# Kernel optimization log

Hardware: AMD Instinct MI355X
Metric: run time of the kernel (lower is better)

The kernel has to match this reference:

```python
import jax, jax.numpy as jnp
import numpy as np

N_NODES = 50000
N_EDGES = 800000
DIM_IN, DIM_H, DIM_OUT = 128, 128, 64


def _init_linear(key, fan_in, fan_out):
    # kaiming-uniform-ish init, matches torch Linear scale
    lim = 1.0 / np.sqrt(fan_in)
    return jax.random.uniform(key, (fan_in, fan_out), jnp.float32, -lim, lim)


def setup_inputs() -> dict:
    key = jax.random.key(0)
    ks = jax.random.split(key, 12)
    x = jax.random.normal(ks[0], (N_NODES, DIM_IN), jnp.float32)
    edge_index = jax.random.randint(ks[1], (2, N_EDGES), 0, N_NODES, jnp.int32)
    dims = [(DIM_IN, DIM_H), (DIM_H, DIM_H), (DIM_H, DIM_OUT)]
    inp = {"x": x, "edge_index": edge_index}
    for i, (fi, fo) in enumerate(dims):
        inp[f"Wl{i}"] = _init_linear(ks[2 + 3 * i], fi, fo)   # neighbor transform
        inp[f"Wr{i}"] = _init_linear(ks[3 + 3 * i], fi, fo)   # root transform
        inp[f"b{i}"] = jnp.zeros((fo,), jnp.float32)
    return inp


def _sage_layer(x, src, dst, Wl, Wr, b):
    # mean aggregation of neighbor messages x[src] at destination nodes
    msg = x[src]                                              # [E, d]
    agg = jax.ops.segment_sum(msg, dst, num_segments=N_NODES)  # [N, d]
    cnt = jax.ops.segment_sum(jnp.ones((src.shape[0],), x.dtype), dst,
                              num_segments=N_NODES)
    mean = agg / jnp.maximum(cnt, 1.0)[:, None]               # isolated nodes -> 0
    return mean @ Wl + b + x @ Wr                              # SAGEConv


def reference(x, edge_index, Wl0, Wr0, b0, Wl1, Wr1, b1, Wl2, Wr2, b2):
    src, dst = edge_index[0], edge_index[1]
    layers = [(Wl0, Wr0, b0), (Wl1, Wr1, b1), (Wl2, Wr2, b2)]
    h = x
    for i, (Wl, Wr, b) in enumerate(layers):
        h = _sage_layer(h, src, dst, Wl, Wr, b)
        if i != len(layers) - 1:
            h = jax.nn.relu(h)  # dropout p=0.2 is identity in eval mode
    return jax.nn.log_softmax(h, axis=1), h
```

## Files before the change

kernel.cpp:

```cpp
#include <hip/hip_runtime.h>

#define N_NODES 50000
#define N_EDGES 800000
#define SCAN_BLOCKS 196
#define WIN 6250

typedef __attribute__((ext_vector_type(8))) short short8;
typedef __attribute__((ext_vector_type(4))) float f32x4;
typedef unsigned short ushort_t;
typedef unsigned int uint_t;

__device__ inline ushort_t f2bf(float f) {
    union { float f; uint_t u; } v; v.f = f;
    uint_t u = v.u;
    u += 0x7fffu + ((u >> 16) & 1u);
    return (ushort_t)(u >> 16);
}
__device__ inline float bflo(uint_t v) { return __uint_as_float(v << 16); }
__device__ inline float bfhi(uint_t v) { return __uint_as_float(v & 0xffff0000u); }
__device__ inline uint_t packbf(float a, float b) {
    return (uint_t)f2bf(a) | ((uint_t)f2bf(b) << 16);
}

__global__ void prep(const float* __restrict__ x, uint_t* __restrict__ x_bf_u,
                     const float* __restrict__ Wl0, const float* __restrict__ Wr0,
                     const float* __restrict__ Wl1, const float* __restrict__ Wr1,
                     const float* __restrict__ Wl2, const float* __restrict__ Wr2,
                     ushort_t* __restrict__ pk0, ushort_t* __restrict__ pk1,
                     ushort_t* __restrict__ pkz, int* __restrict__ cnt) {
    int b = blockIdx.x, tid = threadIdx.x;
    if (b < 6250) {
        int i = b * 256 + tid;
        float4 v = ((const float4*)x)[i];
        x_bf_u[i * 2] = packbf(v.x, v.y);
        x_bf_u[i * 2 + 1] = packbf(v.z, v.w);
    } else if (b < 6506) {
        int bb = b - 6250;
        const float* Wl = (bb < 128) ? Wl0 : Wl1;
        const float* Wr = (bb < 128) ? Wr0 : Wr1;
        ushort_t* out = (bb < 128) ? pk0 : pk1;
        int idx = (bb & 127) * 256 + tid;
        int j = idx & 7, l = (idx >> 3) & 63, t = (idx >> 9) & 7, ks = idx >> 12;
        int n = t * 16 + (l & 15);
        int k = ks * 32 + (l >> 4) * 8 + j;
        float w = (k < 128) ? Wl[k * 128 + n] : Wr[(k - 128) * 128 + n];
        out[idx] = f2bf(w);
    } else if (b < 6570) {
        int idx = (b - 6506) * 256 + tid;
        int j = idx & 7, l = (idx >> 3) & 63, t = (idx >> 9) & 7, ks = idx >> 12;
        int n = t * 16 + (l & 15);
        int k = ks * 32 + (l >> 4) * 8 + j;
        float w = (n < 64) ? Wl2[k * 64 + n] : Wr2[k * 64 + (n - 64)];
        pkz[idx] = f2bf(w);
    } else {
        int i = (b - 6570) * 256 + tid;
        if (i < 12500) ((int4*)cnt)[i] = make_int4(0, 0, 0, 0);
    }
}

__global__ void count_edges_mp(const int* __restrict__ ei, int* __restrict__ cnt) {
    int g = blockIdx.x & 7;
    int nb = gridDim.x >> 3;
    int bi = blockIdx.x >> 3;
    int lo = g * WIN;
    for (int e = bi * 256 + threadIdx.x; e < N_EDGES; e += nb * 256) {
        int d = ei[N_EDGES + e];
        if ((unsigned)(d - lo) < WIN) atomicAdd(&cnt[d], 1);
    }
}

__global__ void fill_csr_mp(const int* __restrict__ ei, int* __restrict__ cursor,
                            int* __restrict__ csr_src) {
    int g = blockIdx.x & 7;
    int nb = gridDim.x >> 3;
    int bi = blockIdx.x >> 3;
    int lo = g * WIN;
    for (int e = bi * 256 + threadIdx.x; e < N_EDGES; e += nb * 256) {
        int d = ei[N_EDGES + e];
        if ((unsigned)(d - lo) < WIN) {
            int p = atomicAdd(&cursor[d], 1);
            csr_src[p] = ei[e];
        }
    }
}

__global__ void scan_all(const int* __restrict__ cnt, int* __restrict__ rowstart,
                         int* __restrict__ cursor) {
    __shared__ int s[256];
    __shared__ int wsum[4];
    int t = threadIdx.x, b = blockIdx.x;
    int base = b * 256;
    int pre = 0;
    for (int i = t; i < base; i += 256) pre += cnt[i];
    for (int off = 32; off; off >>= 1) pre += __shfl_down(pre, off, 64);
    if ((t & 63) == 0) wsum[t >> 6] = pre;
    __syncthreads();
    int prefix_base = wsum[0] + wsum[1] + wsum[2] + wsum[3];
    int i = base + t;
    int v = (i < N_NODES) ? cnt[i] : 0;
    s[t] = v;
    __syncthreads();
    for (int off = 1; off < 256; off <<= 1) {
        int add = (t >= off) ? s[t - off] : 0;
        __syncthreads();
        s[t] += add;
        __syncthreads();
    }
    int excl = s[t] - v + prefix_base;
    if (i < N_NODES) { rowstart[i] = excl; cursor[i] = excl; }
    if (b == 0 && t == 0) rowstart[N_NODES] = N_EDGES;
}

__device__ inline void gather_mean4_128(const uint4* __restrict__ base,
                                        const int* __restrict__ rowstart,
                                        const int* __restrict__ csr,
                                        int node, int lane, float* acc) {
    int s0 = rowstart[node], s1 = rowstart[node + 1];
    #pragma unroll
    for (int k = 0; k < 8; ++k) acc[k] = 0.f;
    int chunk = lane & 15, esel = lane >> 4;
    for (int b = s0; b < s1; b += 64) {
        int m = min(64, s1 - b);
        int idx = (lane < m) ? csr[b + lane] : 0;
        int j = 0;
        for (; j + 16 <= m; j += 16) {
            int i0 = __shfl(idx, j + esel, 64);
            int i1 = __shfl(idx, j + 4 + esel, 64);
            int i2 = __shfl(idx, j + 8 + esel, 64);
            int i3 = __shfl(idx, j + 12 + esel, 64);
            uint4 v0 = base[(size_t)i0 * 16 + chunk];
            uint4 v1 = base[(size_t)i1 * 16 + chunk];
            uint4 v2 = base[(size_t)i2 * 16 + chunk];
            uint4 v3 = base[(size_t)i3 * 16 + chunk];
            acc[0] += (bflo(v0.x) + bflo(v1.x)) + (bflo(v2.x) + bflo(v3.x));
            acc[1] += (bfhi(v0.x) + bfhi(v1.x)) + (bfhi(v2.x) + bfhi(v3.x));
            acc[2] += (bflo(v0.y) + bflo(v1.y)) + (bflo(v2.y) + bflo(v3.y));
            acc[3] += (bfhi(v0.y) + bfhi(v1.y)) + (bfhi(v2.y) + bfhi(v3.y));
            acc[4] += (bflo(v0.z) + bflo(v1.z)) + (bflo(v2.z) + bflo(v3.z));
            acc[5] += (bfhi(v0.z) + bfhi(v1.z)) + (bfhi(v2.z) + bfhi(v3.z));
            acc[6] += (bflo(v0.w) + bflo(v1.w)) + (bflo(v2.w) + bflo(v3.w));
            acc[7] += (bfhi(v0.w) + bfhi(v1.w)) + (bfhi(v2.w) + bfhi(v3.w));
        }
        for (; j < m; j += 4) {
            int e = j + esel;
            int s = __shfl(idx, min(e, m - 1), 64);
            if (e < m) {
                uint4 v = base[(size_t)s * 16 + chunk];
                acc[0] += bflo(v.x); acc[1] += bfhi(v.x);
                acc[2] += bflo(v.y); acc[3] += bfhi(v.y);
                acc[4] += bflo(v.z); acc[5] += bfhi(v.z);
                acc[6] += bflo(v.w); acc[7] += bfhi(v.w);
            }
        }
    }
    float inv = 1.0f / fmaxf((float)(s1 - s0), 1.0f);
    #pragma unroll
    for (int k = 0; k < 8; ++k) {
        acc[k] += __shfl_xor(acc[k], 16, 64);
        acc[k] += __shfl_xor(acc[k], 32, 64);
        acc[k] *= inv;
    }
}

template <bool CHAIN>
__global__ __launch_bounds__(512, 8) void layer_fused(
    const uint4* __restrict__ gsrc, const ushort_t* __restrict__ root,
    const int* __restrict__ rowstart, const int* __restrict__ csr_src,
    const ushort_t* __restrict__ Bpk, const float* __restrict__ bias1,
    const ushort_t* __restrict__ Bpkz, const float* __restrict__ bias2,
    ushort_t* __restrict__ h_out,
    ushort_t* __restrict__ z_bf, float* __restrict__ r_f32) {
    __shared__ __align__(16) ushort_t At[16 * 136];
    int lane = threadIdx.x & 63, wave = threadIdx.x >> 6;
    int nodeBase = blockIdx.x * 16;
    int chunk = lane & 15;

    #pragma unroll
    for (int i = 0; i < 2; ++i) {
        int m = wave * 2 + i;
        int node = nodeBase + m;
        float acc[8];
        #pragma unroll
        for (int k = 0; k < 8; ++k) acc[k] = 0.f;
        if (node < N_NODES) gather_mean4_128(gsrc, rowstart, csr_src, node, lane, acc);
        if (lane < 16) {
            uint4 w;
            w.x = packbf(acc[0], acc[1]); w.y = packbf(acc[2], acc[3]);
            w.z = packbf(acc[4], acc[5]); w.w = packbf(acc[6], acc[7]);
            *(uint4*)&At[m * 136 + chunk * 8] = w;
        }
    }
    __syncthreads();

    int row16 = lane & 15, quad = lane >> 4;
    const short8* bp = (const short8*)Bpk + lane;
    int rootRow = min(nodeBase + row16, N_NODES - 1);
    const ushort_t* rrow = root + (size_t)rootRow * 128;

    f32x4 acc1 = {0.f, 0.f, 0.f, 0.f};
    #pragma unroll
    for (int ks = 0; ks < 8; ++ks) {
        short8 afrag;
        if (ks < 4) afrag = *(const short8*)&At[row16 * 136 + ks * 32 + quad * 8];
        else        afrag = *(const short8*)(rrow + (ks - 4) * 32 + quad * 8);
        short8 bfrag = bp[(ks * 8 + wave) * 64];
        acc1 = __builtin_amdgcn_mfma_f32_16x16x32_bf16(afrag, bfrag, acc1, 0, 0, 0);
    }

    int col = wave * 16 + row16;
    if (!CHAIN) {
        float bv = bias1[col];
        #pragma unroll
        for (int r = 0; r < 4; ++r) {
            int row = nodeBase + quad * 4 + r;
            if (row < N_NODES) {
                float v = fmaxf(acc1[r] + bv, 0.f);
                h_out[(size_t)row * 128 + col] = f2bf(v);
            }
        }
    } else {
        __syncthreads();
        float bv = bias1[col];
        #pragma unroll
        for (int r = 0; r < 4; ++r) {
            float v = fmaxf(acc1[r] + bv, 0.f);
            At[(quad * 4 + r) * 136 + col] = f2bf(v);
        }
        __syncthreads();

        const short8* bpz = (const short8*)Bpkz + lane;
        f32x4 acc2 = {0.f, 0.f, 0.f, 0.f};
        #pragma unroll
        for (int ks = 0; ks < 4; ++ks) {
            short8 afrag = *(const short8*)&At[row16 * 136 + ks * 32 + quad * 8];
            short8 bfrag = bpz[(ks * 8 + wave) * 64];
            acc2 = __builtin_amdgcn_mfma_f32_16x16x32_bf16(afrag, bfrag, acc2, 0, 0, 0);
        }

        #pragma unroll
        for (int r = 0; r < 4; ++r) {
            int row = nodeBase + quad * 4 + r;
            if (row < N_NODES) {
                if (col < 64) z_bf[(size_t)row * 64 + col] = f2bf(acc2[r]);
                else          r_f32[(size_t)row * 64 + (col - 64)] = acc2[r] + bias2[col - 64];
            }
        }
    }
}

__global__ void final_agg_softmax(const uint4* __restrict__ zb,
                                  const float* __restrict__ r_f32,
                                  const int* __restrict__ rowstart,
                                  const int* __restrict__ csr_src,
                                  float* __restrict__ out) {
    int node = blockIdx.x * 4 + (threadIdx.x >> 6);
    int lane = threadIdx.x & 63;
    if (node >= N_NODES) return;
    int s0 = rowstart[node], s1 = rowstart[node + 1];
    int chunk = lane & 7, esel = lane >> 3;
    float acc[8];
    #pragma unroll
    for (int k = 0; k < 8; ++k) acc[k] = 0.f;
    for (int b = s0; b < s1; b += 64) {
        int m = min(64, s1 - b);
        int idx = (lane < m) ? csr_src[b + lane] : 0;
        int j = 0;
        for (; j + 32 <= m; j += 32) {
            int i0 = __shfl(idx, j + esel, 64);
            int i1 = __shfl(idx, j + 8 + esel, 64);
            int i2 = __shfl(idx, j + 16 + esel, 64);
            int i3 = __shfl(idx, j + 24 + esel, 64);
            uint4 v0 = zb[(size_t)i0 * 8 + chunk];
            uint4 v1 = zb[(size_t)i1 * 8 + chunk];
            uint4 v2 = zb[(size_t)i2 * 8 + chunk];
            uint4 v3 = zb[(size_t)i3 * 8 + chunk];
            acc[0] += (bflo(v0.x) + bflo(v1.x)) + (bflo(v2.x) + bflo(v3.x));
            acc[1] += (bfhi(v0.x) + bfhi(v1.x)) + (bfhi(v2.x) + bfhi(v3.x));
            acc[2] += (bflo(v0.y) + bflo(v1.y)) + (bflo(v2.y) + bflo(v3.y));
            acc[3] += (bfhi(v0.y) + bfhi(v1.y)) + (bfhi(v2.y) + bfhi(v3.y));
            acc[4] += (bflo(v0.z) + bflo(v1.z)) + (bflo(v2.z) + bflo(v3.z));
            acc[5] += (bfhi(v0.z) + bfhi(v1.z)) + (bfhi(v2.z) + bfhi(v3.z));
            acc[6] += (bflo(v0.w) + bflo(v1.w)) + (bflo(v2.w) + bflo(v3.w));
            acc[7] += (bfhi(v0.w) + bfhi(v1.w)) + (bfhi(v2.w) + bfhi(v3.w));
        }
        for (; j < m; j += 8) {
            int e = j + esel;
            int s = __shfl(idx, min(e, m - 1), 64);
            if (e < m) {
                uint4 v = zb[(size_t)s * 8 + chunk];
                acc[0] += bflo(v.x); acc[1] += bfhi(v.x);
                acc[2] += bflo(v.y); acc[3] += bfhi(v.y);
                acc[4] += bflo(v.z); acc[5] += bfhi(v.z);
                acc[6] += bflo(v.w); acc[7] += bfhi(v.w);
            }
        }
    }
    float inv = 1.0f / fmaxf((float)(s1 - s0), 1.0f);
    #pragma unroll
    for (int k = 0; k < 8; ++k) {
        acc[k] += __shfl_xor(acc[k], 8, 64);
        acc[k] += __shfl_xor(acc[k], 16, 64);
        acc[k] += __shfl_xor(acc[k], 32, 64);
    }
    const float4* rp = (const float4*)(r_f32 + (size_t)node * 64 + chunk * 8);
    float4 r0 = rp[0], r1 = rp[1];
    float h[8];
    h[0] = acc[0] * inv + r0.x; h[1] = acc[1] * inv + r0.y;
    h[2] = acc[2] * inv + r0.z; h[3] = acc[3] * inv + r0.w;
    h[4] = acc[4] * inv + r1.x; h[5] = acc[5] * inv + r1.y;
    h[6] = acc[6] * inv + r1.z; h[7] = acc[7] * inv + r1.w;
    float mx = h[0];
    #pragma unroll
    for (int k = 1; k < 8; ++k) mx = fmaxf(mx, h[k]);
    mx = fmaxf(mx, __shfl_xor(mx, 1, 64));
    mx = fmaxf(mx, __shfl_xor(mx, 2, 64));
    mx = fmaxf(mx, __shfl_xor(mx, 4, 64));
    float s = 0.f;
    #pragma unroll
    for (int k = 0; k < 8; ++k) s += expf(h[k] - mx);
    s += __shfl_xor(s, 1, 64);
    s += __shfl_xor(s, 2, 64);
    s += __shfl_xor(s, 4, 64);
    float lse = mx + logf(s);
    if (lane < 8) {
        float4* o0 = (float4*)(out + (size_t)node * 64 + chunk * 8);
        float4* o1 = (float4*)(out + (size_t)N_NODES * 64 + (size_t)node * 64 + chunk * 8);
        float4 a = {h[0] - lse, h[1] - lse, h[2] - lse, h[3] - lse};
        float4 bq = {h[4] - lse, h[5] - lse, h[6] - lse, h[7] - lse};
        o0[0] = a; o0[1] = bq;
        float4 c = {h[0], h[1], h[2], h[3]};
        float4 d = {h[4], h[5], h[6], h[7]};
        o1[0] = c; o1[1] = d;
    }
}

extern "C" void kernel_launch(void* const* d_in, const int* in_sizes, int n_in,
                              void* d_out, int out_size, void* d_ws, size_t ws_size,
                              hipStream_t stream) {
    const float* x  = (const float*)d_in[0];
    const int* ei   = (const int*)d_in[1];
    const float* Wl0 = (const float*)d_in[2];
    const float* Wr0 = (const float*)d_in[3];
    const float* b0  = (const float*)d_in[4];
    const float* Wl1 = (const float*)d_in[5];
    const float* Wr1 = (const float*)d_in[6];
    const float* b1  = (const float*)d_in[7];
    const float* Wl2 = (const float*)d_in[8];
    const float* Wr2 = (const float*)d_in[9];
    const float* b2  = (const float*)d_in[10];
    float* out = (float*)d_out;

    char* ws = (char*)d_ws;
    int* cnt      = (int*)(ws + 0x000000);
    int* rowstart = (int*)(ws + 0x040000);
    int* cursor   = (int*)(ws + 0x080000);
    int* csr_src  = (int*)(ws + 0x100000);
    ushort_t* pk0 = (ushort_t*)(ws + 0x420000);
    ushort_t* pk1 = (ushort_t*)(ws + 0x440000);
    ushort_t* pkz = (ushort_t*)(ws + 0x460000);
    ushort_t* x_bf = (ushort_t*)(ws + 0x0500000);
    ushort_t* h1   = (ushort_t*)(ws + 0x1F00000);
    ushort_t* z_bf = (ushort_t*)(ws + 0x1200000);
    float*    r_f32 = (float*)  (ws + 0x0500000);

    prep<<<6619, 256, 0, stream>>>(x, (uint_t*)x_bf, Wl0, Wr0, Wl1, Wr1, Wl2, Wr2,
                                   pk0, pk1, pkz, cnt);

    count_edges_mp<<<1024, 256, 0, stream>>>(ei, cnt);
    scan_all<<<SCAN_BLOCKS, 256, 0, stream>>>(cnt, rowstart, cursor);
    fill_csr_mp<<<1024, 256, 0, stream>>>(ei, cursor, csr_src);

    layer_fused<false><<<3125, 512, 0, stream>>>(
        (const uint4*)x_bf, x_bf, rowstart, csr_src, pk0, b0,
        nullptr, nullptr, h1, nullptr, nullptr);

    layer_fused<true><<<3125, 512, 0, stream>>>(
        (const uint4*)h1, h1, rowstart, csr_src, pk1, b1,
        pkz, b2, nullptr, z_bf, r_f32);

    final_agg_softmax<<<12500, 256, 0, stream>>>((const uint4*)z_bf, r_f32,
                                                 rowstart, csr_src, out);
}
```

Baseline: 337.4 us.

## Gather neighbor features in FP8 instead of BF16 across all three layers

Adds FP8 (e4m3) copies of x, the layer-1 output and the final-layer z projection. All neighbor-gather loops read these 1-byte values instead of BF16, halving the bytes fetched per edge in the memory-bound aggregation. Each lane now handles 16 features, so lane mapping and shuffle reductions are reworked, and the fused layer's launch-bounds occupancy hint drops from 8 to 4. The cost is extra byte-granular stores for the FP8 copies and a noticeable accuracy loss, since values are cast to FP8 without any scaling.

```diff
diff --git a/kernel.cpp b/kernel.cpp
--- a/kernel.cpp
+++ b/kernel.cpp
@@ -7,6 +7,7 @@
 
 typedef __attribute__((ext_vector_type(8))) short short8;
 typedef __attribute__((ext_vector_type(4))) float f32x4;
+typedef __attribute__((ext_vector_type(2))) float f32x2;
 typedef unsigned short ushort_t;
 typedef unsigned int uint_t;
 
@@ -16,13 +17,24 @@
     u += 0x7fffu + ((u >> 16) & 1u);
     return (ushort_t)(u >> 16);
 }
-__device__ inline float bflo(uint_t v) { return __uint_as_float(v << 16); }
-__device__ inline float bfhi(uint_t v) { return __uint_as_float(v & 0xffff0000u); }
 __device__ inline uint_t packbf(float a, float b) {
     return (uint_t)f2bf(a) | ((uint_t)f2bf(b) << 16);
 }
+__device__ inline void acc_fp8x4(uint_t u, float* a) {
+    f32x2 p0 = __builtin_amdgcn_cvt_pk_f32_fp8(u, false);
+    f32x2 p1 = __builtin_amdgcn_cvt_pk_f32_fp8(u, true);
+    a[0] += p0.x; a[1] += p0.y; a[2] += p1.x; a[3] += p1.y;
+}
+__device__ inline void acc_fp8x16(uint4 v, float* a) {
+    acc_fp8x4(v.x, a); acc_fp8x4(v.y, a + 4);
+    acc_fp8x4(v.z, a + 8); acc_fp8x4(v.w, a + 12);
+}
+__device__ inline unsigned char f2fp8(float f) {
+    return (unsigned char)(__builtin_amdgcn_cvt_pk_fp8_f32(f, f, 0, false) & 0xff);
+}
 
 __global__ void prep(const float* __restrict__ x, uint_t* __restrict__ x_bf_u,
+                     uint_t* __restrict__ x_f8_u,
                      const float* __restrict__ Wl0, const float* __restrict__ Wr0,
                      const float* __restrict__ Wl1, const float* __restrict__ Wr1,
                      const float* __restrict__ Wl2, const float* __restrict__ Wr2,
@@ -34,6 +46,9 @@
         float4 v = ((const float4*)x)[i];
         x_bf_u[i * 2] = packbf(v.x, v.y);
         x_bf_u[i * 2 + 1] = packbf(v.z, v.w);
+        uint_t u = __builtin_amdgcn_cvt_pk_fp8_f32(v.x, v.y, 0, false);
+        u = __builtin_amdgcn_cvt_pk_fp8_f32(v.z, v.w, u, true);
+        x_f8_u[i] = u;
     } else if (b < 6506) {
         int bb = b - 6250;
         const float* Wl = (bb < 128) ? Wl0 : Wl1;
@@ -111,51 +126,37 @@
     if (b == 0 && t == 0) rowstart[N_NODES] = N_EDGES;
 }
 
-__device__ inline void gather_mean4_128(const uint4* __restrict__ base,
-                                        const int* __restrict__ rowstart,
-                                        const int* __restrict__ csr,
-                                        int node, int lane, float* acc) {
+__device__ inline void gather_mean_fp8_128(const uint4* __restrict__ base,
+                                           const int* __restrict__ rowstart,
+                                           const int* __restrict__ csr,
+                                           int node, int lane, float* acc) {
     int s0 = rowstart[node], s1 = rowstart[node + 1];
-    #pragma unroll
-    for (int k = 0; k < 8; ++k) acc[k] = 0.f;
-    int chunk = lane & 15, esel = lane >> 4;
+    int chunk = lane & 7, esel = lane >> 3;
     for (int b = s0; b < s1; b += 64) {
         int m = min(64, s1 - b);
         int idx = (lane < m) ? csr[b + lane] : 0;
         int j = 0;
         for (; j + 16 <= m; j += 16) {
             int i0 = __shfl(idx, j + esel, 64);
-            int i1 = __shfl(idx, j + 4 + esel, 64);
-            int i2 = __shfl(idx, j + 8 + esel, 64);
-            int i3 = __shfl(idx, j + 12 + esel, 64);
-            uint4 v0 = base[(size_t)i0 * 16 + chunk];
-            uint4 v1 = base[(size_t)i1 * 16 + chunk];
-            uint4 v2 = base[(size_t)i2 * 16 + chunk];
-            uint4 v3 = base[(size_t)i3 * 16 + chunk];
-            acc[0] += (bflo(v0.x) + bflo(v1.x)) + (bflo(v2.x) + bflo(v3.x));
-            acc[1] += (bfhi(v0.x) + bfhi(v1.x)) + (bfhi(v2.x) + bfhi(v3.x));
-            acc[2] += (bflo(v0.y) + bflo(v1.y)) + (bflo(v2.y) + bflo(v3.y));
-            acc[3] += (bfhi(v0.y) + bfhi(v1.y)) + (bfhi(v2.y) + bfhi(v3.y));
-            acc[4] += (bflo(v0.z) + bflo(v1.z)) + (bflo(v2.z) + bflo(v3.z));
-            acc[5] += (bfhi(v0.z) + bfhi(v1.z)) + (bfhi(v2.z) + bfhi(v3.z));
-            acc[6] += (bflo(v0.w) + bflo(v1.w)) + (bflo(v2.w) + bflo(v3.w));
-            acc[7] += (bfhi(v0.w) + bfhi(v1.w)) + (bfhi(v2.w) + bfhi(v3.w));
-        }
-        for (; j < m; j += 4) {
+            int i1 = __shfl(idx, j + 8 + esel, 64);
+            uint4 v0 = base[(size_t)i0 * 8 + chunk];
+            uint4 v1 = base[(size_t)i1 * 8 + chunk];
+            acc_fp8x16(v0, acc);
+            acc_fp8x16(v1, acc);
+        }
+        for (; j < m; j += 8) {
             int e = j + esel;
             int s = __shfl(idx, min(e, m - 1), 64);
             if (e < m) {
-                uint4 v = base[(size_t)s * 16 + chunk];
-                acc[0] += bflo(v.x); acc[1] += bfhi(v.x);
-                acc[2] += bflo(v.y); acc[3] += bfhi(v.y);
-                acc[4] += bflo(v.z); acc[5] += bfhi(v.z);
-                acc[6] += bflo(v.w); acc[7] += bfhi(v.w);
+                uint4 v = base[(size_t)s * 8 + chunk];
+                acc_fp8x16(v, acc);
             }
         }
     }
     float inv = 1.0f / fmaxf((float)(s1 - s0), 1.0f);
     #pragma unroll
-    for (int k = 0; k < 8; ++k) {
+    for (int k = 0; k < 16; ++k) {
+        acc[k] += __shfl_xor(acc[k], 8, 64);
         acc[k] += __shfl_xor(acc[k], 16, 64);
         acc[k] += __shfl_xor(acc[k], 32, 64);
         acc[k] *= inv;
@@ -163,31 +164,35 @@
 }
 
 template <bool CHAIN>
-__global__ __launch_bounds__(512, 8) void layer_fused(
-    const uint4* __restrict__ gsrc, const ushort_t* __restrict__ root,
+__global__ __launch_bounds__(512, 4) void layer_fused(
+    const uint4* __restrict__ gsrc_f8, const ushort_t* __restrict__ root,
     const int* __restrict__ rowstart, const int* __restrict__ csr_src,
     const ushort_t* __restrict__ Bpk, const float* __restrict__ bias1,
     const ushort_t* __restrict__ Bpkz, const float* __restrict__ bias2,
-    ushort_t* __restrict__ h_out,
-    ushort_t* __restrict__ z_bf, float* __restrict__ r_f32) {
+    ushort_t* __restrict__ h_out, unsigned char* __restrict__ h_out_f8,
+    unsigned char* __restrict__ z_f8, float* __restrict__ r_f32) {
     __shared__ __align__(16) ushort_t At[16 * 136];
     int lane = threadIdx.x & 63, wave = threadIdx.x >> 6;
     int nodeBase = blockIdx.x * 16;
-    int chunk = lane & 15;
+    int chunk = lane & 7;
 
     #pragma unroll
     for (int i = 0; i < 2; ++i) {
         int m = wave * 2 + i;
         int node = nodeBase + m;
-        float acc[8];
-        #pragma unroll
-        for (int k = 0; k < 8; ++k) acc[k] = 0.f;
-        if (node < N_NODES) gather_mean4_128(gsrc, rowstart, csr_src, node, lane, acc);
-        if (lane < 16) {
-            uint4 w;
-            w.x = packbf(acc[0], acc[1]); w.y = packbf(acc[2], acc[3]);
-            w.z = packbf(acc[4], acc[5]); w.w = packbf(acc[6], acc[7]);
-            *(uint4*)&At[m * 136 + chunk * 8] = w;
+        float acc[16];
+        #pragma unroll
+        for (int k = 0; k < 16; ++k) acc[k] = 0.f;
+        if (node < N_NODES)
+            gather_mean_fp8_128(gsrc_f8, rowstart, csr_src, node, lane, acc);
+        if (lane < 8) {
+            uint4 w0, w1;
+            w0.x = packbf(acc[0], acc[1]);  w0.y = packbf(acc[2], acc[3]);
+            w0.z = packbf(acc[4], acc[5]);  w0.w = packbf(acc[6], acc[7]);
+            w1.x = packbf(acc[8], acc[9]);  w1.y = packbf(acc[10], acc[11]);
+            w1.z = packbf(acc[12], acc[13]); w1.w = packbf(acc[14], acc[15]);
+            *(uint4*)&At[m * 136 + chunk * 16] = w0;
+            *(uint4*)&At[m * 136 + chunk * 16 + 8] = w1;
         }
     }
     __syncthreads();
@@ -216,6 +221,7 @@
             if (row < N_NODES) {
                 float v = fmaxf(acc1[r] + bv, 0.f);
                 h_out[(size_t)row * 128 + col] = f2bf(v);
+                h_out_f8[(size_t)row * 128 + col] = f2fp8(v);
             }
         }
     } else {
@@ -241,14 +247,14 @@
         for (int r = 0; r < 4; ++r) {
             int row = nodeBase + quad * 4 + r;
             if (row < N_NODES) {
-                if (col < 64) z_bf[(size_t)row * 64 + col] = f2bf(acc2[r]);
+                if (col < 64) z_f8[(size_t)row * 64 + col] = f2fp8(acc2[r]);
                 else          r_f32[(size_t)row * 64 + (col - 64)] = acc2[r] + bias2[col - 64];
             }
         }
     }
 }
 
-__global__ void final_agg_softmax(const uint4* __restrict__ zb,
+__global__ void final_agg_softmax(const uint4* __restrict__ zb_f8,
                                   const float* __restrict__ r_f32,
                                   const int* __restrict__ rowstart,
                                   const int* __restrict__ csr_src,
@@ -257,80 +263,72 @@
     int lane = threadIdx.x & 63;
     if (node >= N_NODES) return;
     int s0 = rowstart[node], s1 = rowstart[node + 1];
-    int chunk = lane & 7, esel = lane >> 3;
-    float acc[8];
-    #pragma unroll
-    for (int k = 0; k < 8; ++k) acc[k] = 0.f;
+    int chunk = lane & 3, esel = lane >> 2;
+    float acc[16];
+    #pragma unroll
+    for (int k = 0; k < 16; ++k) acc[k] = 0.f;
     for (int b = s0; b < s1; b += 64) {
         int m = min(64, s1 - b);
         int idx = (lane < m) ? csr_src[b + lane] : 0;
         int j = 0;
         for (; j + 32 <= m; j += 32) {
             int i0 = __shfl(idx, j + esel, 64);
-            int i1 = __shfl(idx, j + 8 + esel, 64);
-            int i2 = __shfl(idx, j + 16 + esel, 64);
-            int i3 = __shfl(idx, j + 24 + esel, 64);
-            uint4 v0 = zb[(size_t)i0 * 8 + chunk];
-            uint4 v1 = zb[(size_t)i1 * 8 + chunk];
-            uint4 v2 = zb[(size_t)i2 * 8 + chunk];
-            uint4 v3 = zb[(size_t)i3 * 8 + chunk];
-            acc[0] += (bflo(v0.x) + bflo(v1.x)) + (bflo(v2.x) + bflo(v3.x));
-            acc[1] += (bfhi(v0.x) + bfhi(v1.x)) + (bfhi(v2.x) + bfhi(v3.x));
-            acc[2] += (bflo(v0.y) + bflo(v1.y)) + (bflo(v2.y) + bflo(v3.y));
-            acc[3] += (bfhi(v0.y) + bfhi(v1.y)) + (bfhi(v2.y) + bfhi(v3.y));
-            acc[4] += (bflo(v0.z) + bflo(v1.z)) + (bflo(v2.z) + bflo(v3.z));
-            acc[5] += (bfhi(v0.z) + bfhi(v1.z)) + (bfhi(v2.z) + bfhi(v3.z));
-            acc[6] += (bflo(v0.w) + bflo(v1.w)) + (bflo(v2.w) + bflo(v3.w));
-            acc[7] += (bfhi(v0.w) + bfhi(v1.w)) + (bfhi(v2.w) + bfhi(v3.w));
-        }
-        for (; j < m; j += 8) {
+            int i1 = __shfl(idx, j + 16 + esel, 64);
+            uint4 v0 = zb_f8[(size_t)i0 * 4 + chunk];
+            uint4 v1 = zb_f8[(size_t)i1 * 4 + chunk];
+            acc_fp8x16(v0, acc);
+            acc_fp8x16(v1, acc);
+        }
+        for (; j < m; j += 16) {
             int e = j + esel;
             int s = __shfl(idx, min(e, m - 1), 64);
             if (e < m) {
-                uint4 v = zb[(size_t)s * 8 + chunk];
-                acc[0] += bflo(v.x); acc[1] += bfhi(v.x);
-                acc[2] += bflo(v.y); acc[3] += bfhi(v.y);
-                acc[4] += bflo(v.z); acc[5] += bfhi(v.z);
-                acc[6] += bflo(v.w); acc[7] += bfhi(v.w);
+                uint4 v = zb_f8[(size_t)s * 4 + chunk];
+                acc_fp8x16(v, acc);
             }
         }
     }
     float inv = 1.0f / fmaxf((float)(s1 - s0), 1.0f);
     #pragma unroll
-    for (int k = 0; k < 8; ++k) {
+    for (int k = 0; k < 16; ++k) {
+        acc[k] += __shfl_xor(acc[k], 4, 64);
         acc[k] += __shfl_xor(acc[k], 8, 64);
         acc[k] += __shfl_xor(acc[k], 16, 64);
         acc[k] += __shfl_xor(acc[k], 32, 64);
     }
-    const float4* rp = (const float4*)(r_f32 + (size_t)node * 64 + chunk * 8);
-    float4 r0 = rp[0], r1 = rp[1];
-    float h[8];
-    h[0] = acc[0] * inv + r0.x; h[1] = acc[1] * inv + r0.y;
-    h[2] = acc[2] * inv + r0.z; h[3] = acc[3] * inv + r0.w;
-    h[4] = acc[4] * inv + r1.x; h[5] = acc[5] * inv + r1.y;
-    h[6] = acc[6] * inv + r1.z; h[7] = acc[7] * inv + r1.w;
+    float h[16];
+    {
+        const float4* rp = (const float4*)(r_f32 + (size_t)node * 64 + chunk * 16);
+        #pragma unroll
+        for (int q = 0; q < 4; ++q) {
+            float4 rv = rp[q];
+            h[q * 4 + 0] = acc[q * 4 + 0] * inv + rv.x;
+            h[q * 4 + 1] = acc[q * 4 + 1] * inv + rv.y;
+            h[q * 4 + 2] = acc[q * 4 + 2] * inv + rv.z;
+            h[q * 4 + 3] = acc[q * 4 + 3] * inv + rv.w;
+        }
+    }
     float mx = h[0];
     #pragma unroll
-    for (int k = 1; k < 8; ++k) mx = fmaxf(mx, h[k]);
+    for (int k = 1; k < 16; ++k) mx = fmaxf(mx, h[k]);
     mx = fmaxf(mx, __shfl_xor(mx, 1, 64));
     mx = fmaxf(mx, __shfl_xor(mx, 2, 64));
-    mx = fmaxf(mx, __shfl_xor(mx, 4, 64));
     float s = 0.f;
     #pragma unroll
-    for (int k = 0; k < 8; ++k) s += expf(h[k] - mx);
+    for (int k = 0; k < 16; ++k) s += expf(h[k] - mx);
     s += __shfl_xor(s, 1, 64);
     s += __shfl_xor(s, 2, 64);
-    s += __shfl_xor(s, 4, 64);
     float lse = mx + logf(s);
-    if (lane < 8) {
-        float4* o0 = (float4*)(out + (size_t)node * 64 + chunk * 8);
-        float4* o1 = (float4*)(out + (size_t)N_NODES * 64 + (size_t)node * 64 + chunk * 8);
-        float4 a = {h[0] - lse, h[1] - lse, h[2] - lse, h[3] - lse};
-        float4 bq = {h[4] - lse, h[5] - lse, h[6] - lse, h[7] - lse};
-        o0[0] = a; o0[1] = bq;
-        float4 c = {h[0], h[1], h[2], h[3]};
-        float4 d = {h[4], h[5], h[6], h[7]};
-        o1[0] = c; o1[1] = d;
+    if (lane < 4) {
+        float4* o0 = (float4*)(out + (size_t)node * 64 + chunk * 16);
+        float4* o1 = (float4*)(out + (size_t)N_NODES * 64 + (size_t)node * 64 + chunk * 16);
+        #pragma unroll
+        for (int q = 0; q < 4; ++q) {
+            float4 a = {h[q * 4 + 0] - lse, h[q * 4 + 1] - lse,
+                        h[q * 4 + 2] - lse, h[q * 4 + 3] - lse};
+            float4 c = {h[q * 4 + 0], h[q * 4 + 1], h[q * 4 + 2], h[q * 4 + 3]};
+            o0[q] = a; o1[q] = c;
+        }
     }
 }
 
@@ -360,10 +358,13 @@
     ushort_t* pkz = (ushort_t*)(ws + 0x460000);
     ushort_t* x_bf = (ushort_t*)(ws + 0x0500000);
     ushort_t* h1   = (ushort_t*)(ws + 0x1F00000);
-    ushort_t* z_bf = (ushort_t*)(ws + 0x1200000);
-    float*    r_f32 = (float*)  (ws + 0x0500000);
-
-    prep<<<6619, 256, 0, stream>>>(x, (uint_t*)x_bf, Wl0, Wr0, Wl1, Wr1, Wl2, Wr2,
+    unsigned char* x_f8 = (unsigned char*)(ws + 0x2C00000);
+    unsigned char* h1_f8 = (unsigned char*)(ws + 0x3400000);
+    unsigned char* z_f8  = (unsigned char*)(ws + 0x3C00000);
+    float* r_f32 = (float*)(ws + 0x0500000);
+
+    prep<<<6619, 256, 0, stream>>>(x, (uint_t*)x_bf, (uint_t*)x_f8,
+                                   Wl0, Wr0, Wl1, Wr1, Wl2, Wr2,
                                    pk0, pk1, pkz, cnt);
 
     count_edges_mp<<<1024, 256, 0, stream>>>(ei, cnt);
@@ -371,13 +372,13 @@
     fill_csr_mp<<<1024, 256, 0, stream>>>(ei, cursor, csr_src);
 
     layer_fused<false><<<3125, 512, 0, stream>>>(
-        (const uint4*)x_bf, x_bf, rowstart, csr_src, pk0, b0,
-        nullptr, nullptr, h1, nullptr, nullptr);
+        (const uint4*)x_f8, x_bf, rowstart, csr_src, pk0, b0,
+        nullptr, nullptr, h1, h1_f8, nullptr, nullptr);
 
     layer_fused<true><<<3125, 512, 0, stream>>>(
-        (const uint4*)h1, h1, rowstart, csr_src, pk1, b1,
-        pkz, b2, nullptr, z_bf, r_f32);
-
-    final_agg_softmax<<<12500, 256, 0, stream>>>((const uint4*)z_bf, r_f32,
+        (const uint4*)h1_f8, h1, rowstart, csr_src, pk1, b1,
+        pkz, b2, nullptr, nullptr, z_f8, r_f32);
+
+    final_agg_softmax<<<12500, 256, 0, stream>>>((const uint4*)z_f8, r_f32,
                                                  rowstart, csr_src, out);
 }
```

After: 346.5 us. 2.7% more time.
